# Performance work log

Hardware: AMD Instinct MI355X
Metric: run time of the kernel (lower is better)

Reference implementation:

```python
import jax, jax.numpy as jnp
import numpy as np

WINDOW_SIZE = 11
N_CHANNELS = 3
SIGMA = 1.5
K1, K2 = 0.01, 0.03
VALUE_RANGE = 1.0


def _create_window(window_size: int, n_channels: int, sigma: float) -> np.ndarray:
    # 1D gaussian, normalized, then outer product -> 2D kernel
    coords = np.arange(window_size, dtype=np.float32) - (window_size - 1) / 2.0
    g = np.exp(-(coords ** 2) / (2.0 * sigma ** 2))
    g = g / g.sum()
    k2d = np.outer(g, g).astype(np.float32)  # (K, K), sums to 1
    # depthwise kernel, OIHW with I=1 (groups = n_channels)
    return np.broadcast_to(k2d, (n_channels, 1, window_size, window_size)).copy()


def _dwconv(x, window):
    # depthwise valid conv, NCHW / OIHW
    return jax.lax.conv_general_dilated(
        x, window, window_strides=(1, 1), padding='VALID',
        feature_group_count=window.shape[0],
        dimension_numbers=('NCHW', 'OIHW', 'NCHW'))


def setup_inputs() -> dict:
    key = jax.random.key(0)
    kx, ky = jax.random.split(key)
    N, C, H, W = 32, N_CHANNELS, 512, 512
    x = jax.random.uniform(kx, (N, C, H, W), dtype=jnp.float32)
    y = jax.random.uniform(ky, (N, C, H, W), dtype=jnp.float32)
    window = jnp.asarray(_create_window(WINDOW_SIZE, N_CHANNELS, SIGMA))
    return {"x": x, "y": y, "window": window}


def reference(x, y, window):
    c1 = (K1 * VALUE_RANGE) ** 2
    c2 = (K2 * VALUE_RANGE) ** 2

    mu_x = _dwconv(x, window)
    mu_y = _dwconv(y, window)
    mu_x_sq = mu_x ** 2
    mu_y_sq = mu_y ** 2
    mu_xy = mu_x * mu_y

    sigma_x_sq = _dwconv(x * x, window) - mu_x_sq
    sigma_y_sq = _dwconv(y * y, window) - mu_y_sq
    sigma_xy = _dwconv(x * y, window) - mu_xy

    cs = (2.0 * sigma_xy + c2) / (sigma_x_sq + sigma_y_sq + c2)
    ss = (2.0 * mu_xy + c1) / (mu_x_sq + mu_y_sq + c1) * cs

    l = ss.mean(axis=(-1, -2))  # (N, C) per-channel SSIM
    l = l.mean(axis=-1)         # (N,)  per-sample
    return l.mean()             # reduction='mean'
```

## Files before the change

kernel.cpp:

```cpp
#include <hip/hip_runtime.h>

typedef float v2f __attribute__((ext_vector_type(2)));

#define KS    11
#define HH    512
#define WW    512
#define OUTD  502
#define OH    34
#define GR    11
#define NG    4
#define NBR   15
#define NBC   2
#define TC    256
#define CH    67
#define SGL   268
#define NIMG  96
#define ITEMS (GR * CH)

__device__ __forceinline__ v2f pk_fma(v2f a, v2f b, v2f c) {
    v2f d;
    asm("v_pk_fma_f32 %0, %1, %2, %3" : "=v"(d) : "v"(a), "v"(b), "v"(c));
    return d;
}
__device__ __forceinline__ v2f pk_mul(v2f a, v2f b) {
    v2f d;
    asm("v_pk_mul_f32 %0, %1, %2" : "=v"(d) : "v"(a), "v"(b));
    return d;
}

__global__ __launch_bounds__(256, 3)
void ssim_main(const float* __restrict__ xg, const float* __restrict__ yg,
               const float* __restrict__ win, double* __restrict__ acc_out)
{
    __shared__ v2f buf[GR][SGL];
    __shared__ float wsums[4];

    const int tid = threadIdx.x;
    int bb = blockIdx.x;
    const int img  = bb % NIMG;  bb /= NIMG;
    const int band = bb % NBR;   bb /= NBR;
    const int cb   = bb * TC;
    const int row0 = band * OH;

    v2f g2[6];
    #pragma unroll
    for (int i = 0; i < 6; i++) {
        float s = 0.f;
        #pragma unroll
        for (int j = 0; j < KS; j++) s += win[i * KS + j];
        v2f p; p.x = s; p.y = s; g2[i] = p;
    }

    const float* xi = xg + (size_t)img * (HH * WW);
    const float* yi = yg + (size_t)img * (HH * WW);

    float4 pfx[3], pfy[3];
    auto prefetch = [&](int g) {
        #pragma unroll
        for (int it = 0; it < 3; it++) {
            const int idx = tid + 256 * it;
            if (it < 2 || idx < ITEMS) {
                int i = idx / CH, k = idx - i * CH;
                int gr = row0 + g * GR + i; if (gr > HH - 1) gr = HH - 1;
                int gc = cb + 4 * k;        if (gc > WW - 4) gc = WW - 4;
                const size_t base = (size_t)gr * WW + gc;
                pfx[it] = *(const float4*)(xi + base);
                pfy[it] = *(const float4*)(yi + base);
            }
        }
    };
    auto store_s = [&]() {
        #pragma unroll
        for (int it = 0; it < 3; it++) {
            const int idx = tid + 256 * it;
            if (it < 2 || idx < ITEMS) {
                int i = idx / CH, k = idx - i * CH;
                const float4 xv = pfx[it], yv = pfy[it];
                float4 a; a.x = xv.x; a.y = yv.x; a.z = xv.y; a.w = yv.y;
                float4 b; b.x = xv.z; b.y = yv.z; b.z = xv.w; b.w = yv.w;
                *(float4*)&buf[i][4 * k]     = a;
                *(float4*)&buf[i][4 * k + 2] = b;
            }
        }
    };

    v2f aMu[KS], aSq[KS]; float aXy[KS];
    #pragma unroll
    for (int s = 0; s < KS; s++) { aMu[s] = (v2f)0.f; aSq[s] = (v2f)0.f; aXy[s] = 0.f; }

    float ssum = 0.f;
    const float C1 = 0.0001f;
    const float C2 = 0.0009f;
    const bool colvalid = (cb + tid) < OUTD;

    prefetch(0); store_s(); prefetch(1);
    __syncthreads();

    #pragma unroll 1
    for (int g = 0; g < NG; g++) {
        #pragma unroll
        for (int rr = 0; rr < GR; rr++) {
            const v2f* rowp = &buf[rr][tid];

            v2f hMu = (v2f)0.f, hSq = (v2f)0.f; float hXy = 0.f;
            #pragma unroll
            for (int j = 0; j < KS; j++) {
                const v2f gj = g2[j < 6 ? j : 10 - j];
                const v2f v = rowp[j];
                hMu = pk_fma(gj, v, hMu);
                hSq = pk_fma(gj, pk_mul(v, v), hSq);
                hXy = fmaf(gj.x, v.x * v.y, hXy);
            }

            #pragma unroll
            for (int i = 0; i < KS; i++) {
                const int slot = (rr - i + KS) % KS;
                const v2f gi = g2[i < 6 ? i : 10 - i];
                aMu[slot] = pk_fma(gi, hMu, aMu[slot]);
                aSq[slot] = pk_fma(gi, hSq, aSq[slot]);
                aXy[slot] = fmaf(gi.x, hXy, aXy[slot]);
            }

            const int es   = (rr + 1) % KS;
            const int r    = g * GR + rr;
            const int jloc = r - (KS - 1);
            if (jloc >= 0 && (row0 + jloc) < OUTD && colvalid) {
                const float mx  = aMu[es].x, my  = aMu[es].y;
                const float Sxx = aSq[es].x, Syy = aSq[es].y, Sxy = aXy[es];
                const float mxx = mx * mx, myy = my * my, mxy = mx * my;
                const float sxx = Sxx - mxx, syy = Syy - myy, sxy = Sxy - mxy;
                const float num = (2.f * mxy + C1) * (2.f * sxy + C2);
                const float den = (mxx + myy + C1) * (sxx + syy + C2);
                float rc = __builtin_amdgcn_rcpf(den);
                rc = rc * fmaf(-den, rc, 2.0f);
                ssum = fmaf(num, rc, ssum);
            }
            aMu[es] = (v2f)0.f; aSq[es] = (v2f)0.f; aXy[es] = 0.f;
        }

        __syncthreads();
        if (g < NG - 1) {
            store_s();
            __syncthreads();
            if (g < NG - 2) prefetch(g + 2);
        }
    }

    #pragma unroll
    for (int off = 32; off > 0; off >>= 1)
        ssum += __shfl_down(ssum, off);
    const int wave = tid >> 6;
    if ((tid & 63) == 0) wsums[wave] = ssum;
    __syncthreads();
    if (tid == 0) {
        float s = wsums[0] + wsums[1] + wsums[2] + wsums[3];
        atomicAdd(acc_out, (double)s);
    }
}

__global__ void ssim_finalize(const double* __restrict__ acc, float* __restrict__ out)
{
    out[0] = (float)(acc[0] * (1.0 / 24192384.0));
}

extern "C" void kernel_launch(void* const* d_in, const int* in_sizes, int n_in,
                              void* d_out, int out_size, void* d_ws, size_t ws_size,
                              hipStream_t stream)
{
    const float* x   = (const float*)d_in[0];
    const float* y   = (const float*)d_in[1];
    const float* win = (const float*)d_in[2];
    float* out = (float*)d_out;
    double* acc = (double*)d_ws;

    hipMemsetAsync(acc, 0, sizeof(double), stream);
    ssim_main<<<dim3(NIMG * NBR * NBC), dim3(256), 0, stream>>>(x, y, win, acc);
    ssim_finalize<<<dim3(1), dim3(1), 0, stream>>>(acc, out);
}
```

Before: 285.2 us.

## Double-buffer LDS row groups, taller bands, and ring-buffered separable vertical pass

Bands grow from 34 to 45 output rows (12 bands, 5 groups of 11 rows), so each block spends a smaller share of its loaded rows on the 10-row halo. The LDS tile becomes double-buffered, which leaves one barrier per group instead of two. The horizontal pass now keeps four per-row sums (x, y, x²+y², xy) in an 11-row ring buffer, and each output row gets a full 11-tap vertical pass instead of scattered accumulations into 11 slots. Global loads switch from float4 to float2 and the packed-FMA inline asm is dropped. The costs are twice the LDS (which may affect 3 blocks/CU occupancy), more vertical-pass FMAs and register pressure, and narrower global loads.

```diff
diff --git a/kernel.cpp b/kernel.cpp
--- a/kernel.cpp
+++ b/kernel.cpp
@@ -6,33 +6,24 @@
 #define HH    512
 #define WW    512
 #define OUTD  502
-#define OH    34
 #define GR    11
-#define NG    4
-#define NBR   15
+#define NG    5
+#define ROWS  55
+#define OH    45
+#define NBR   12
 #define NBC   2
 #define TC    256
-#define CH    67
+#define SGQ   134
 #define SGL   268
 #define NIMG  96
-#define ITEMS (GR * CH)
-
-__device__ __forceinline__ v2f pk_fma(v2f a, v2f b, v2f c) {
-    v2f d;
-    asm("v_pk_fma_f32 %0, %1, %2, %3" : "=v"(d) : "v"(a), "v"(b), "v"(c));
-    return d;
-}
-__device__ __forceinline__ v2f pk_mul(v2f a, v2f b) {
-    v2f d;
-    asm("v_pk_mul_f32 %0, %1, %2" : "=v"(d) : "v"(a), "v"(b));
-    return d;
-}
+#define ITEMS (GR * SGQ)
+#define NIT   6
 
 __global__ __launch_bounds__(256, 3)
 void ssim_main(const float* __restrict__ xg, const float* __restrict__ yg,
                const float* __restrict__ win, double* __restrict__ acc_out)
 {
-    __shared__ v2f buf[GR][SGL];
+    __shared__ v2f buf[2][GR][SGL];
     __shared__ float wsums[4];
 
     const int tid = threadIdx.x;
@@ -42,108 +33,119 @@
     const int cb   = bb * TC;
     const int row0 = band * OH;
 
-    v2f g2[6];
+    float g[KS];
     #pragma unroll
-    for (int i = 0; i < 6; i++) {
+    for (int i = 0; i < KS; i++) {
         float s = 0.f;
         #pragma unroll
         for (int j = 0; j < KS; j++) s += win[i * KS + j];
-        v2f p; p.x = s; p.y = s; g2[i] = p;
+        g[i] = s;
     }
 
     const float* xi = xg + (size_t)img * (HH * WW);
     const float* yi = yg + (size_t)img * (HH * WW);
 
-    float4 pfx[3], pfy[3];
-    auto prefetch = [&](int g) {
+    float2 pfx[NIT], pfy[NIT];
+    auto prefetch = [&](int gidx) {
         #pragma unroll
-        for (int it = 0; it < 3; it++) {
+        for (int it = 0; it < NIT; it++) {
             const int idx = tid + 256 * it;
-            if (it < 2 || idx < ITEMS) {
-                int i = idx / CH, k = idx - i * CH;
-                int gr = row0 + g * GR + i; if (gr > HH - 1) gr = HH - 1;
-                int gc = cb + 4 * k;        if (gc > WW - 4) gc = WW - 4;
+            if (idx < ITEMS) {
+                int i = idx / SGQ, k = idx - i * SGQ;
+                int gr = row0 + gidx * GR + i; if (gr > HH - 1) gr = HH - 1;
+                int gc = cb + 2 * k;           if (gc > WW - 2) gc = WW - 2;
                 const size_t base = (size_t)gr * WW + gc;
-                pfx[it] = *(const float4*)(xi + base);
-                pfy[it] = *(const float4*)(yi + base);
+                pfx[it] = *(const float2*)(xi + base);
+                pfy[it] = *(const float2*)(yi + base);
             }
         }
     };
-    auto store_s = [&]() {
+    auto store_s = [&](int bsel) {
         #pragma unroll
-        for (int it = 0; it < 3; it++) {
+        for (int it = 0; it < NIT; it++) {
             const int idx = tid + 256 * it;
-            if (it < 2 || idx < ITEMS) {
-                int i = idx / CH, k = idx - i * CH;
-                const float4 xv = pfx[it], yv = pfy[it];
-                float4 a; a.x = xv.x; a.y = yv.x; a.z = xv.y; a.w = yv.y;
-                float4 b; b.x = xv.z; b.y = yv.z; b.z = xv.w; b.w = yv.w;
-                *(float4*)&buf[i][4 * k]     = a;
-                *(float4*)&buf[i][4 * k + 2] = b;
+            if (idx < ITEMS) {
+                int i = idx / SGQ, k = idx - i * SGQ;
+                float4 w; w.x = pfx[it].x; w.y = pfy[it].x;
+                          w.z = pfx[it].y; w.w = pfy[it].y;
+                *(float4*)&buf[bsel][i][2 * k] = w;
             }
         }
     };
 
-    v2f aMu[KS], aSq[KS]; float aXy[KS];
+    float rh[4][KS];
     #pragma unroll
-    for (int s = 0; s < KS; s++) { aMu[s] = (v2f)0.f; aSq[s] = (v2f)0.f; aXy[s] = 0.f; }
+    for (int q = 0; q < 4; q++)
+        #pragma unroll
+        for (int s = 0; s < KS; s++) rh[q][s] = 0.f;
 
     float ssum = 0.f;
     const float C1 = 0.0001f;
     const float C2 = 0.0009f;
     const bool colvalid = (cb + tid) < OUTD;
 
-    prefetch(0); store_s(); prefetch(1);
+    auto hpass = [&](const v2f* rowp, int rr) {
+        float hx = 0.f, hy = 0.f, hs = 0.f, hp = 0.f;
+        #pragma unroll
+        for (int j = 0; j < KS; j++) {
+            const v2f v = rowp[j];
+            const float s = fmaf(v.y, v.y, v.x * v.x);
+            const float p = v.x * v.y;
+            hx = fmaf(g[j], v.x, hx);
+            hy = fmaf(g[j], v.y, hy);
+            hs = fmaf(g[j], s,   hs);
+            hp = fmaf(g[j], p,   hp);
+        }
+        rh[0][rr] = hx; rh[1][rr] = hy; rh[2][rr] = hs; rh[3][rr] = hp;
+    };
+    auto vpass = [&](int rr, int jout) {
+        float mx = 0.f, my = 0.f, S = 0.f, P = 0.f;
+        #pragma unroll
+        for (int i = 0; i < KS; i++) {
+            const int sl = (rr + 1 + i) % KS;
+            mx = fmaf(g[i], rh[0][sl], mx);
+            my = fmaf(g[i], rh[1][sl], my);
+            S  = fmaf(g[i], rh[2][sl], S);
+            P  = fmaf(g[i], rh[3][sl], P);
+        }
+        if (jout < OUTD && colvalid) {
+            const float mxx = mx * mx, myy = my * my, mxy = mx * my;
+            const float ssig = S - mxx - myy;
+            const float sxy  = P - mxy;
+            const float num = (2.f * mxy + C1) * (2.f * sxy + C2);
+            const float den = (mxx + myy + C1) * (ssig + C2);
+            float rc = __builtin_amdgcn_rcpf(den);
+            rc = rc * fmaf(-den, rc, 2.0f);
+            ssum = fmaf(num, rc, ssum);
+        }
+    };
+
+    prefetch(0); store_s(0); prefetch(1);
     __syncthreads();
 
-    #pragma unroll 1
-    for (int g = 0; g < NG; g++) {
+    {
+        store_s(1);
+        prefetch(2);
+        const v2f (*bufc)[SGL] = buf[0];
         #pragma unroll
         for (int rr = 0; rr < GR; rr++) {
-            const v2f* rowp = &buf[rr][tid];
-
-            v2f hMu = (v2f)0.f, hSq = (v2f)0.f; float hXy = 0.f;
-            #pragma unroll
-            for (int j = 0; j < KS; j++) {
-                const v2f gj = g2[j < 6 ? j : 10 - j];
-                const v2f v = rowp[j];
-                hMu = pk_fma(gj, v, hMu);
-                hSq = pk_fma(gj, pk_mul(v, v), hSq);
-                hXy = fmaf(gj.x, v.x * v.y, hXy);
-            }
-
-            #pragma unroll
-            for (int i = 0; i < KS; i++) {
-                const int slot = (rr - i + KS) % KS;
-                const v2f gi = g2[i < 6 ? i : 10 - i];
-                aMu[slot] = pk_fma(gi, hMu, aMu[slot]);
-                aSq[slot] = pk_fma(gi, hSq, aSq[slot]);
-                aXy[slot] = fmaf(gi.x, hXy, aXy[slot]);
-            }
-
-            const int es   = (rr + 1) % KS;
-            const int r    = g * GR + rr;
-            const int jloc = r - (KS - 1);
-            if (jloc >= 0 && (row0 + jloc) < OUTD && colvalid) {
-                const float mx  = aMu[es].x, my  = aMu[es].y;
-                const float Sxx = aSq[es].x, Syy = aSq[es].y, Sxy = aXy[es];
-                const float mxx = mx * mx, myy = my * my, mxy = mx * my;
-                const float sxx = Sxx - mxx, syy = Syy - myy, sxy = Sxy - mxy;
-                const float num = (2.f * mxy + C1) * (2.f * sxy + C2);
-                const float den = (mxx + myy + C1) * (sxx + syy + C2);
-                float rc = __builtin_amdgcn_rcpf(den);
-                rc = rc * fmaf(-den, rc, 2.0f);
-                ssum = fmaf(num, rc, ssum);
-            }
-            aMu[es] = (v2f)0.f; aSq[es] = (v2f)0.f; aXy[es] = 0.f;
+            hpass(&bufc[rr][tid], rr);
+            if (rr == GR - 1) vpass(rr, row0);
         }
-
         __syncthreads();
-        if (g < NG - 1) {
-            store_s();
-            __syncthreads();
-            if (g < NG - 2) prefetch(g + 2);
+    }
+    #pragma unroll 1
+    for (int gi = 1; gi < NG; gi++) {
+        if (gi + 1 < NG) store_s((gi + 1) & 1);
+        if (gi + 2 < NG) prefetch(gi + 2);
+        const v2f (*bufc)[SGL] = buf[gi & 1];
+        const int jbase = row0 + gi * GR - (KS - 1);
+        #pragma unroll
+        for (int rr = 0; rr < GR; rr++) {
+            hpass(&bufc[rr][tid], rr);
+            vpass(rr, jbase + rr);
         }
+        __syncthreads();
     }
 
     #pragma unroll
```

Result: slower. 316.9 us (+11.1%).
